# Performance work log

Hardware: AMD Instinct MI355X
Metric: run time of the kernel (lower is better)

Reference implementation:

```python
import jax, jax.numpy as jnp
import numpy as np

CONTEXT_DIM = 64
HIDDEN = 512
BS = 1024
SEQ = 168
TWIN = 96


def setup_inputs() -> dict:
    key = jax.random.key(0)
    k0, k1, k2, k3 = jax.random.split(key, 4)
    x_dyn = jax.random.normal(k0, (BS, SEQ, CONTEXT_DIM), jnp.float32)
    y_flow = jax.random.normal(k1, (BS, SEQ, 1), jnp.float32)
    input_dim = CONTEXT_DIM + 1 + 1
    W = jax.random.normal(k2, (input_dim + HIDDEN, HIDDEN * 4), jnp.float32) * 0.02
    b = jnp.zeros((HIDDEN * 4,), jnp.float32)
    Wo = jax.random.normal(k3, (HIDDEN, 1), jnp.float32) * 0.02
    bo = jnp.zeros((1,), jnp.float32)
    return {"x_dyn": x_dyn, "y_flow": y_flow, "W": W, "b": b,
            "Wo": Wo, "bo": bo, "twin_idx": TWIN}


def _cell(inp, h, c, W, b, hidden):
    # fused gate GEMM: [bs, input_dim+hidden] @ [input_dim+hidden, 4*hidden]
    gates = jnp.concatenate([inp, h], axis=1) @ W + b
    i, f, g, o = jnp.split(gates, 4, axis=1)
    i = jax.nn.sigmoid(i)
    f = jax.nn.sigmoid(f)
    o = jax.nn.sigmoid(o)
    g = jnp.tanh(g)
    c_next = f * c + i * g
    h_next = o * jnp.tanh(c_next)
    return h_next, c_next


def reference(x_dyn, y_flow, W, b, Wo, bo, twin_idx):
    bs, seq_len, _ = x_dyn.shape
    hidden = W.shape[1] // 4
    h0 = jnp.zeros((bs, hidden), x_dyn.dtype)
    c0 = jnp.zeros((bs, hidden), x_dyn.dtype)
    zeros_col = jnp.zeros((bs, 1), x_dyn.dtype)
    ones_col = jnp.ones((bs, 1), x_dyn.dtype)

    # Phase 1: teacher-forced steps t in [0, twin_idx), h_since_tw = 0
    def step1(carry, xs):
        h, c = carry
        x_t, y_t = xs
        inp = jnp.concatenate([x_t, y_t, zeros_col], axis=1)
        h, c = _cell(inp, h, c, W, b, hidden)
        pred = h @ Wo + bo  # [bs, 1]
        return (h, c), pred

    xs1 = (jnp.swapaxes(x_dyn[:, :twin_idx], 0, 1),
           jnp.swapaxes(y_flow[:, :twin_idx], 0, 1))
    (h, c), preds1 = jax.lax.scan(step1, (h0, c0), xs1)  # preds1: [twin_idx, bs, 1]
    last_out = preds1[-1]

    n2 = seq_len - 1 - twin_idx
    h_vals = (jnp.arange(n2, dtype=x_dyn.dtype) + 1.0) / 24.0

    def step2(carry, xs):
        h, c, last = carry
        x_t, hv = xs
        inp = jnp.concatenate([x_t, last, hv * ones_col], axis=1)
        h, c = _cell(inp, h, c, W, b, hidden)
        last = h @ Wo + bo
        return (h, c, last), last

    xs2 = (jnp.swapaxes(x_dyn[:, twin_idx:seq_len - 1], 0, 1), h_vals)
    _, preds2 = jax.lax.scan(step2, (h, c, last_out), xs2)  # [n2, bs, 1]

    preds = jnp.concatenate([preds1, preds2], axis=0)  # [seq_len-1, bs, 1]
    return jnp.swapaxes(preds, 0, 1)  # [bs, seq_len-1, 1]
```

## Files before the change

### kernel.cpp

```cpp
#include <hip/hip_runtime.h>


#define HIDDEN 512
#define SEQ    168
#define NSTEP  167
#define BS     1024
#define CTX    64
#define KM     576
#define KP     584
#define MTILE  128
#define SGRID  512
#define PGRID  256
#define NTHR   256

typedef __attribute__((ext_vector_type(8))) short s16x8;
typedef __attribute__((ext_vector_type(4))) float f32x4;

static __device__ __forceinline__ unsigned short bf16_rne(float f) {
    union { float f; unsigned int u; } v; v.f = f;
    unsigned int r = v.u + 0x7FFFu + ((v.u >> 16) & 1u);
    return (unsigned short)(r >> 16);
}
static __device__ __forceinline__ float bf16_to_f(unsigned short h) {
    union { float f; unsigned int u; } v; v.u = ((unsigned int)h) << 16;
    return v.f;
}
static __device__ __forceinline__ float sigmoid_(float x) {
    x = fminf(fmaxf(x, -80.f), 80.f);
    return 1.0f / (1.0f + __expf(-x));
}
static __device__ __forceinline__ float tanh_(float x) {
    float ax = fminf(fabsf(x), 40.f);
    float e = __expf(-2.0f * ax);
    float r = (1.0f - e) / (1.0f + e);
    return copysignf(r, x);
}

__global__ void lstm_prep(const float* __restrict__ x_dyn, float* __restrict__ out,
                          const float* __restrict__ bo_p,
                          unsigned short* __restrict__ aHi, unsigned short* __restrict__ aLo,
                          float* __restrict__ cst)
{
    const int gthr = blockIdx.x * NTHR + threadIdx.x;
    const int gstr = PGRID * NTHR;
    const float bo = *bo_p;
    for (int i = gthr; i < BS * NSTEP; i += gstr) out[i] = bo;
    for (int i = gthr; i < BS * HIDDEN; i += gstr) cst[i] = 0.f;
    for (int i = gthr; i < BS * 256; i += gstr) {
        const int b = i >> 8, j = i & 255;
        ((unsigned int*)aHi)[b * 288 + 32 + j] = 0u;
        ((unsigned int*)aLo)[b * 288 + 32 + j] = 0u;
    }
    for (int i = gthr; i < BS * CTX; i += gstr) {
        const int b = i >> 6, col = i & 63;
        const float v = x_dyn[(size_t)b * SEQ * CTX + col];
        const unsigned short hi = bf16_rne(v);
        aHi[(size_t)b * KM + col] = hi;
        aLo[(size_t)b * KM + col] = bf16_rne(v - bf16_to_f(hi));
    }
}

__global__ __launch_bounds__(NTHR, 2)
void lstm_step(const float* __restrict__ x_dyn, const float* __restrict__ y_flow,
               const float* __restrict__ Wg, const float* __restrict__ bias,
               const float* __restrict__ Wo, const int* __restrict__ twin_p,
               float* __restrict__ out, unsigned short* __restrict__ aHi,
               unsigned short* __restrict__ aLo, float* __restrict__ cst, int t)
{
    extern __shared__ unsigned char smem_raw[];
    unsigned short* whi = (unsigned short*)smem_raw;
    unsigned short* wlo = whi + 32 * KP;
    float* a64s = (float*)(wlo + 32 * KP);

    const int tid = threadIdx.x, bid = blockIdx.x;
    const int nt = bid >> 3;
    const int m0 = (bid & 7) * MTILE;
    const int lane = tid & 63, wv = tid >> 6;
    const int ln15 = lane & 15, kg = lane >> 4;
    const int twin = *twin_p;

    const int par = t & 1, pn = par ^ 1;
    const unsigned short* aH = aHi + (size_t)par * BS * KM;
    const unsigned short* aL = aLo + (size_t)par * BS * KM;
    unsigned short* nH = aHi + (size_t)pn * BS * KM;
    unsigned short* nL = aLo + (size_t)pn * BS * KM;
    const float hv = (t < twin) ? 0.f : (float)(t - twin + 1) * (1.f / 24.f);

    for (int idx = tid; idx < 32 * KM; idx += NTHR) {
        const int k = idx >> 5, c = idx & 31;
        const int wrow = (k < 64) ? k : (k + 2);
        const int wcol = (2 * (c >> 4) + ((c >> 3) & 1)) * 512 + nt * 8 + (c & 7);
        const float v = Wg[(size_t)wrow * 2048 + wcol];
        const unsigned short hi = bf16_rne(v);
        whi[c * KP + k] = hi;
        wlo[c * KP + k] = bf16_rne(v - bf16_to_f(hi));
    }

    if (tid < MTILE) {
        const int b = m0 + tid;
        float v;
        if (t < twin) v = y_flow[(size_t)b * SEQ + t];
        else if (t > 0) v = out[(size_t)b * NSTEP + (t - 1)];
        else v = 0.f;
        a64s[tid] = v;
    }
    __syncthreads();

    if (tid < 128) {
        const int b = m0 + nt * 2 + (tid >> 6), col = tid & 63;
        const float v = x_dyn[((size_t)b * SEQ + (t + 1)) * CTX + col];
        const unsigned short hi = bf16_rne(v);
        nH[(size_t)b * KM + col] = hi;
        nL[(size_t)b * KM + col] = bf16_rne(v - bf16_to_f(hi));
    }

    float w64c[2], basec[2];
    #pragma unroll
    for (int ns = 0; ns < 2; ++ns) {
        const int wcol = (2 * ns + (ln15 >> 3)) * 512 + nt * 8 + (ln15 & 7);
        w64c[ns]  = Wg[(size_t)64 * 2048 + wcol];
        basec[ns] = fmaf(hv, Wg[(size_t)65 * 2048 + wcol], bias[wcol]);
    }
    const int u = nt * 8 + (ln15 & 7);
    const float wo_u = Wo[u];
    const bool lo_half = (ln15 < 8);

    const size_t aoff0 = (size_t)(m0 + wv * 32 + ln15) * KM + kg * 8;
    const size_t aoff1 = aoff0 + (size_t)16 * KM;

    f32x4 acc[2][2];
    #pragma unroll
    for (int ms = 0; ms < 2; ++ms)
        #pragma unroll
        for (int ns = 0; ns < 2; ++ns) acc[ms][ns] = (f32x4){0.f, 0.f, 0.f, 0.f};

    s16x8 ah[2][2], al[2][2];
    ah[0][0] = *(const s16x8*)(aH + aoff0);
    ah[0][1] = *(const s16x8*)(aH + aoff1);
    al[0][0] = *(const s16x8*)(aL + aoff0);
    al[0][1] = *(const s16x8*)(aL + aoff1);

    #pragma unroll
    for (int kc = 0; kc < 18; ++kc) {
        const int cur = kc & 1, nxt = cur ^ 1;
        const int k0 = kc * 32;
        if (kc < 17) {
            ah[nxt][0] = *(const s16x8*)(aH + aoff0 + k0 + 32);
            ah[nxt][1] = *(const s16x8*)(aH + aoff1 + k0 + 32);
            al[nxt][0] = *(const s16x8*)(aL + aoff0 + k0 + 32);
            al[nxt][1] = *(const s16x8*)(aL + aoff1 + k0 + 32);
        }
        s16x8 bh[2], bl[2];
        #pragma unroll
        for (int ns = 0; ns < 2; ++ns) {
            const int boff = (ns * 16 + ln15) * KP + k0 + kg * 8;
            bh[ns] = *(const s16x8*)(whi + boff);
            bl[ns] = *(const s16x8*)(wlo + boff);
        }
        #pragma unroll
        for (int ns = 0; ns < 2; ++ns)
            #pragma unroll
            for (int ms = 0; ms < 2; ++ms) {
                acc[ms][ns] = __builtin_amdgcn_mfma_f32_16x16x32_bf16(ah[cur][ms], bh[ns], acc[ms][ns], 0, 0, 0);
                acc[ms][ns] = __builtin_amdgcn_mfma_f32_16x16x32_bf16(ah[cur][ms], bl[ns], acc[ms][ns], 0, 0, 0);
                acc[ms][ns] = __builtin_amdgcn_mfma_f32_16x16x32_bf16(al[cur][ms], bh[ns], acc[ms][ns], 0, 0, 0);
            }
    }

    #pragma unroll
    for (int ms = 0; ms < 2; ++ms) {
        #pragma unroll
        for (int r = 0; r < 4; ++r) {
            const int rl = wv * 32 + ms * 16 + kg * 4 + r;
            const int b = m0 + rl;
            const float a64v = a64s[rl];
            const float pre0 = acc[ms][0][r] + fmaf(a64v, w64c[0], basec[0]);
            const float pre1 = acc[ms][1][r] + fmaf(a64v, w64c[1], basec[1]);
            const float q0 = __shfl_xor(pre0, 8, 16);
            const float q1 = __shfl_xor(pre1, 8, 16);
            const float pi = lo_half ? pre0 : q0;
            const float pf = lo_half ? q0 : pre0;
            const float pg = lo_half ? pre1 : q1;
            const float po = lo_half ? q1 : pre1;
            const float i_ = sigmoid_(pi);
            const float f_ = sigmoid_(pf);
            const float g_ = tanh_(pg);
            const float o_ = sigmoid_(po);
            const size_t ci = (size_t)b * HIDDEN + u;
            const float c = f_ * cst[ci] + i_ * g_;
            const float h = o_ * tanh_(c);
            if (lo_half) {
                cst[ci] = c;
                const unsigned short hh = bf16_rne(h);
                nH[(size_t)b * KM + 64 + u] = hh;
                nL[(size_t)b * KM + 64 + u] = bf16_rne(h - bf16_to_f(hh));
            }
            float p = lo_half ? h * wo_u : 0.f;
            p += __shfl_xor(p, 1, 16);
            p += __shfl_xor(p, 2, 16);
            p += __shfl_xor(p, 4, 16);
            p += __shfl_xor(p, 8, 16);
            if (ln15 == 0) atomicAdd(&out[(size_t)b * NSTEP + t], p);
        }
    }
}

extern "C" void kernel_launch(void* const* d_in, const int* in_sizes, int n_in,
                              void* d_out, int out_size, void* d_ws, size_t ws_size,
                              hipStream_t stream) {
    (void)in_sizes; (void)n_in; (void)out_size; (void)ws_size;
    const float* x_dyn  = (const float*)d_in[0];
    const float* y_flow = (const float*)d_in[1];
    const float* Wg     = (const float*)d_in[2];
    const float* bias   = (const float*)d_in[3];
    const float* Wo     = (const float*)d_in[4];
    const float* bo     = (const float*)d_in[5];
    const int*   twin   = (const int*)d_in[6];
    float* out = (float*)d_out;

    unsigned short* aHi = (unsigned short*)d_ws;
    unsigned short* aLo = aHi + (size_t)2 * BS * KM;
    float* cst = (float*)(aLo + (size_t)2 * BS * KM);

    const unsigned int smem = (2u * 32u * KP) * 2u + MTILE * 4u;

    (void)hipFuncSetAttribute((const void*)lstm_step,
                              hipFuncAttributeMaxDynamicSharedMemorySize, (int)smem);

    lstm_prep<<<dim3(PGRID), dim3(NTHR), 0, stream>>>(x_dyn, out, bo, aHi, aLo, cst);

    for (int t = 0; t < NSTEP; ++t) {
        lstm_step<<<dim3(SGRID), dim3(NTHR), smem, stream>>>(
            x_dyn, y_flow, Wg, bias, Wo, twin, out, aHi, aLo, cst, t);
    }
}
```

Measured before the change: 5.884 ms.

## Pre-split weights once into bf16 hi/lo layout and stream them into LDS

Adds a one-time wprep kernel that converts the gate weights into bf16 hi/lo pairs, stored in the per-tile LDS layout in workspace. Each step kernel then copies its slice with direct global-to-LDS loads instead of gathering strided fp32 weights and converting them on every one of the 167 launches. It also changes the A-operand loading to issue all loads for nine k-chunks up front before the MFMAs, in place of one-ahead double buffering. The cost is extra workspace, higher register pressure from the bulk A loads, and reliance on global_load_lds behaving correctly with the chosen offsets.

Result: faster. 5.099 ms (-13.3%).

```diff
diff --git a/kernel.cpp b/kernel.cpp
--- a/kernel.cpp
+++ b/kernel.cpp
@@ -12,6 +12,7 @@
 #define SGRID  512
 #define PGRID  256
 #define NTHR   256
+#define WTELEM (2 * 32 * KP)
 
 typedef __attribute__((ext_vector_type(8))) short s16x8;
 typedef __attribute__((ext_vector_type(4))) float f32x4;
@@ -60,12 +61,35 @@
     }
 }
 
+__global__ void wprep(const float* __restrict__ Wg, unsigned short* __restrict__ wpl)
+{
+    const int gthr = blockIdx.x * NTHR + threadIdx.x;
+    const int gstr = PGRID * NTHR;
+    for (int i = gthr; i < 64 * 32 * KP; i += gstr) {
+        const int kp = i % KP;
+        const int c  = (i / KP) & 31;
+        const int nt = i / (KP * 32);
+        unsigned short hi = 0, lo = 0;
+        if (kp < KM) {
+            const int wrow = (kp < 64) ? kp : (kp + 2);
+            const int wcol = (2 * (c >> 4) + ((c >> 3) & 1)) * 512 + nt * 8 + (c & 7);
+            const float v = Wg[(size_t)wrow * 2048 + wcol];
+            hi = bf16_rne(v);
+            lo = bf16_rne(v - bf16_to_f(hi));
+        }
+        const size_t base = (size_t)nt * WTELEM + (size_t)c * KP + kp;
+        wpl[base] = hi;
+        wpl[base + 32 * KP] = lo;
+    }
+}
+
 __global__ __launch_bounds__(NTHR, 2)
 void lstm_step(const float* __restrict__ x_dyn, const float* __restrict__ y_flow,
                const float* __restrict__ Wg, const float* __restrict__ bias,
                const float* __restrict__ Wo, const int* __restrict__ twin_p,
                float* __restrict__ out, unsigned short* __restrict__ aHi,
-               unsigned short* __restrict__ aLo, float* __restrict__ cst, int t)
+               unsigned short* __restrict__ aLo, float* __restrict__ cst,
+               const unsigned short* __restrict__ wpl, int t)
 {
     extern __shared__ unsigned char smem_raw[];
     unsigned short* whi = (unsigned short*)smem_raw;
@@ -86,15 +110,19 @@
     unsigned short* nL = aLo + (size_t)pn * BS * KM;
     const float hv = (t < twin) ? 0.f : (float)(t - twin + 1) * (1.f / 24.f);
 
-    for (int idx = tid; idx < 32 * KM; idx += NTHR) {
-        const int k = idx >> 5, c = idx & 31;
-        const int wrow = (k < 64) ? k : (k + 2);
-        const int wcol = (2 * (c >> 4) + ((c >> 3) & 1)) * 512 + nt * 8 + (c & 7);
-        const float v = Wg[(size_t)wrow * 2048 + wcol];
-        const unsigned short hi = bf16_rne(v);
-        whi[c * KP + k] = hi;
-        wlo[c * KP + k] = bf16_rne(v - bf16_to_f(hi));
-    }
+    const unsigned short* wsrc = wpl + (size_t)nt * WTELEM;
+#if __has_builtin(__builtin_amdgcn_global_load_lds)
+    for (int c = wv; c < 73; c += 4) {
+        __builtin_amdgcn_global_load_lds(
+            (const __attribute__((address_space(1))) void*)(wsrc + c * 512 + lane * 8),
+            (__attribute__((address_space(3))) void*)(smem_raw + c * 1024),
+            16, 0, 0);
+    }
+#else
+    for (int idx = tid; idx < WTELEM / 8; idx += NTHR) {
+        *(s16x8*)((unsigned short*)smem_raw + idx * 8) = *(const s16x8*)(wsrc + idx * 8);
+    }
+#endif
 
     if (tid < MTILE) {
         const int b = m0 + tid;
@@ -134,37 +162,36 @@
         #pragma unroll
         for (int ns = 0; ns < 2; ++ns) acc[ms][ns] = (f32x4){0.f, 0.f, 0.f, 0.f};
 
-    s16x8 ah[2][2], al[2][2];
-    ah[0][0] = *(const s16x8*)(aH + aoff0);
-    ah[0][1] = *(const s16x8*)(aH + aoff1);
-    al[0][0] = *(const s16x8*)(aL + aoff0);
-    al[0][1] = *(const s16x8*)(aL + aoff1);
-
-    #pragma unroll
-    for (int kc = 0; kc < 18; ++kc) {
-        const int cur = kc & 1, nxt = cur ^ 1;
-        const int k0 = kc * 32;
-        if (kc < 17) {
-            ah[nxt][0] = *(const s16x8*)(aH + aoff0 + k0 + 32);
-            ah[nxt][1] = *(const s16x8*)(aH + aoff1 + k0 + 32);
-            al[nxt][0] = *(const s16x8*)(aL + aoff0 + k0 + 32);
-            al[nxt][1] = *(const s16x8*)(aL + aoff1 + k0 + 32);
-        }
-        s16x8 bh[2], bl[2];
-        #pragma unroll
-        for (int ns = 0; ns < 2; ++ns) {
-            const int boff = (ns * 16 + ln15) * KP + k0 + kg * 8;
-            bh[ns] = *(const s16x8*)(whi + boff);
-            bl[ns] = *(const s16x8*)(wlo + boff);
-        }
-        #pragma unroll
-        for (int ns = 0; ns < 2; ++ns)
+    #pragma unroll
+    for (int half = 0; half < 2; ++half) {
+        s16x8 Ah[9][2], Al[9][2];
+        #pragma unroll
+        for (int j = 0; j < 9; ++j) {
+            const size_t k0 = (size_t)(half * 9 + j) * 32;
+            Ah[j][0] = *(const s16x8*)(aH + aoff0 + k0);
+            Ah[j][1] = *(const s16x8*)(aH + aoff1 + k0);
+            Al[j][0] = *(const s16x8*)(aL + aoff0 + k0);
+            Al[j][1] = *(const s16x8*)(aL + aoff1 + k0);
+        }
+        #pragma unroll
+        for (int j = 0; j < 9; ++j) {
+            const int k0 = (half * 9 + j) * 32;
+            s16x8 bh[2], bl[2];
             #pragma unroll
-            for (int ms = 0; ms < 2; ++ms) {
-                acc[ms][ns] = __builtin_amdgcn_mfma_f32_16x16x32_bf16(ah[cur][ms], bh[ns], acc[ms][ns], 0, 0, 0);
-                acc[ms][ns] = __builtin_amdgcn_mfma_f32_16x16x32_bf16(ah[cur][ms], bl[ns], acc[ms][ns], 0, 0, 0);
-                acc[ms][ns] = __builtin_amdgcn_mfma_f32_16x16x32_bf16(al[cur][ms], bh[ns], acc[ms][ns], 0, 0, 0);
+            for (int ns = 0; ns < 2; ++ns) {
+                const int boff = (ns * 16 + ln15) * KP + k0 + kg * 8;
+                bh[ns] = *(const s16x8*)(whi + boff);
+                bl[ns] = *(const s16x8*)(wlo + boff);
             }
+            #pragma unroll
+            for (int ns = 0; ns < 2; ++ns)
+                #pragma unroll
+                for (int ms = 0; ms < 2; ++ms) {
+                    acc[ms][ns] = __builtin_amdgcn_mfma_f32_16x16x32_bf16(Ah[j][ms], bh[ns], acc[ms][ns], 0, 0, 0);
+                    acc[ms][ns] = __builtin_amdgcn_mfma_f32_16x16x32_bf16(Ah[j][ms], bl[ns], acc[ms][ns], 0, 0, 0);
+                    acc[ms][ns] = __builtin_amdgcn_mfma_f32_16x16x32_bf16(Al[j][ms], bh[ns], acc[ms][ns], 0, 0, 0);
+                }
+        }
     }
 
     #pragma unroll
@@ -221,6 +248,7 @@
     unsigned short* aHi = (unsigned short*)d_ws;
     unsigned short* aLo = aHi + (size_t)2 * BS * KM;
     float* cst = (float*)(aLo + (size_t)2 * BS * KM);
+    unsigned short* wpl = (unsigned short*)(cst + (size_t)BS * HIDDEN);
 
     const unsigned int smem = (2u * 32u * KP) * 2u + MTILE * 4u;
 
@@ -228,9 +256,10 @@
                               hipFuncAttributeMaxDynamicSharedMemorySize, (int)smem);
 
     lstm_prep<<<dim3(PGRID), dim3(NTHR), 0, stream>>>(x_dyn, out, bo, aHi, aLo, cst);
+    wprep<<<dim3(PGRID), dim3(NTHR), 0, stream>>>(Wg, wpl);
 
     for (int t = 0; t < NSTEP; ++t) {
         lstm_step<<<dim3(SGRID), dim3(NTHR), smem, stream>>>(
-            x_dyn, y_flow, Wg, bias, Wo, twin, out, aHi, aLo, cst, t);
-    }
-}
+            x_dyn, y_flow, Wg, bias, Wo, twin, out, aHi, aLo, cst, wpl, t);
+    }
+}
```
